# Optimization experiments

Measured on AMD Instinct MI355X. Metric: run time of the kernel, lower is better.

Reference implementation:

```python
import jax, jax.numpy as jnp
import numpy as np

HEADS = 8
DIM_HEAD = 64
WINDOW = 256
CAUSAL = True


def _sliding_window_mask(seq_len: int, window: int, causal: bool) -> jnp.ndarray:
    i = jnp.arange(seq_len)[:, None]
    j = jnp.arange(seq_len)[None, :]
    # attend iff i - window + 1 <= j <= i + window - 1 (end_pos exclusive)
    mask = (j >= i - window + 1) & (j <= i + window - 1)
    if causal:
        mask = mask & (j <= i)
    return mask  # (S, S) bool


def setup_inputs() -> dict:
    key = jax.random.key(0)
    k1, k2, k3 = jax.random.split(key, 3)
    dim = 512
    inner = HEADS * DIM_HEAD
    x = jax.random.normal(k1, (2, 2048, dim), dtype=jnp.float32)
    W_qkv = jax.random.normal(k2, (dim, 3 * inner), dtype=jnp.float32) * 0.02
    W_out = jax.random.normal(k3, (inner, dim), dtype=jnp.float32) * 0.02
    return {"x": x, "W_qkv": W_qkv, "W_out": W_out}


def reference(x, W_qkv, W_out):
    B, S, D = x.shape
    H, Dh = HEADS, DIM_HEAD
    scale = Dh ** (-0.5)
    qkv = x @ W_qkv  # (B, S, 3*H*Dh)
    q, k, v = jnp.split(qkv, 3, axis=-1)
    q = q.reshape(B, S, H, Dh).transpose(0, 2, 1, 3)  # (B, H, S, Dh)
    k = k.reshape(B, S, H, Dh).transpose(0, 2, 1, 3)
    v = v.reshape(B, S, H, Dh).transpose(0, 2, 1, 3)
    scores = jnp.einsum('bhid,bhjd->bhij', q, k) * scale
    mask = _sliding_window_mask(S, WINDOW, CAUSAL)
    mask_value = -jnp.finfo(scores.dtype).max
    scores = jnp.where(mask[None, None, :, :], scores, mask_value)
    attn = jax.nn.softmax(scores, axis=-1)  # (B, H, S, S)
    out = jnp.einsum('bhij,bhjd->bhid', attn, v)
    out = out.transpose(0, 2, 1, 3).reshape(B, S, H * Dh)
    out = out @ W_out  # (B, S, D)
    return (out, attn)
```

## Files before the change

### kernel.cpp

```cpp
#include <hip/hip_runtime.h>
#include <hip/hip_bf16.h>

typedef __bf16 bf16x8 __attribute__((ext_vector_type(8)));
typedef __bf16 bf16x4 __attribute__((ext_vector_type(4)));
typedef float f32x4 __attribute__((ext_vector_type(4)));

#define MFMA16(a,b,c) __builtin_amdgcn_mfma_f32_16x16x32_bf16(a, b, c, 0, 0, 0)

__device__ inline void fill_attn_rows(float* __restrict__ attn, int rowStart, int rowEnd,
                                      int tid) {
  const f32x4 z4 = {0.f, 0.f, 0.f, 0.f};
  for (int g = rowStart; g < rowEnd; g++) {
    const int bh = g >> 11, i = g & 2047;
    const int qt = i >> 6;
    const int lo = qt >= 4 ? (qt - 4) << 6 : 0;
    const int hi = (qt + 1) << 6;
    float* rp = attn + ((size_t)bh << 22) + ((size_t)i << 11);
    for (int j = tid << 2; j < lo; j += 1024)
      __builtin_nontemporal_store(z4, reinterpret_cast<f32x4*>(rp + j));
    for (int j = hi + (tid << 2); j < 2048; j += 1024)
      __builtin_nontemporal_store(z4, reinterpret_cast<f32x4*>(rp + j));
  }
}

__device__ inline void fill_block_chunk(float* __restrict__ attn, int fillStart, int fillEnd,
                                        int fid, int nfill, int tid) {
  const int total = fillEnd - fillStart;
  const int per = (total + nfill - 1) / nfill;
  const int myStart = fillStart + fid * per;
  int myEnd = myStart + per;
  if (myEnd > fillEnd) myEnd = fillEnd;
  if (myStart < myEnd) fill_attn_rows(attn, myStart, myEnd, tid);
}

__device__ inline void transpose_body(const float* __restrict__ in, __bf16* __restrict__ out,
                                      int R, int C, int tile, int tid, float (*t)[65]) {
  const int tilesC = C >> 6;
  const int tc = tile % tilesC, tr = tile / tilesC;
  const int r0 = tr << 6, c0 = tc << 6;
  const int ri = tid >> 2, cq = (tid & 3) << 4;
#pragma unroll
  for (int e = 0; e < 16; e += 4) {
    float4 v = *reinterpret_cast<const float4*>(&in[(size_t)(r0 + ri) * C + c0 + cq + e]);
    t[ri][cq + e]     = v.x;
    t[ri][cq + e + 1] = v.y;
    t[ri][cq + e + 2] = v.z;
    t[ri][cq + e + 3] = v.w;
  }
  __syncthreads();
  const int co = tid >> 2, rq = (tid & 3) << 4;
  __attribute__((aligned(16))) __bf16 buf[16];
#pragma unroll
  for (int e = 0; e < 16; e++) buf[e] = (__bf16)t[rq + e][co];
  *reinterpret_cast<bf16x8*>(&out[(size_t)(c0 + co) * R + r0 + rq])     = *reinterpret_cast<bf16x8*>(&buf[0]);
  *reinterpret_cast<bf16x8*>(&out[(size_t)(c0 + co) * R + r0 + rq + 8]) = *reinterpret_cast<bf16x8*>(&buf[8]);
}

__global__ __launch_bounds__(256) void prep(const float* __restrict__ Wqkv,
                                            const float* __restrict__ Wout,
                                            __bf16* __restrict__ Wqt,
                                            __bf16* __restrict__ Wot) {
  __shared__ float t[64][65];
  const int bid = blockIdx.x, tid = threadIdx.x;
  if (bid < 192) transpose_body(Wqkv, Wqt, 512, 1536, bid, tid, t);
  else           transpose_body(Wout, Wot, 512, 512, bid - 192, tid, t);
}

template <typename AT, typename OT>
__global__ __launch_bounds__(256) void gemm_bt(const AT* __restrict__ A,
                                               const __bf16* __restrict__ Bt,
                                               OT* __restrict__ C, int M, int N, int K,
                                               float* __restrict__ fillAttn,
                                               int fillStart, int fillEnd, int gxCompute) {
  __shared__ __bf16 As[128][72];
  __shared__ __bf16 Bs[128][72];
  const int tid = threadIdx.x;

  if ((int)blockIdx.x >= gxCompute) {
    const int nfx = gridDim.x - gxCompute;
    const int fid = (blockIdx.x - gxCompute) + nfx * blockIdx.y;
    fill_block_chunk(fillAttn, fillStart, fillEnd, fid, nfx * gridDim.y, tid);
    return;
  }

  const int wave = tid >> 6, lane = tid & 63;
  const int c = lane & 15, q4 = lane >> 4;
  const int bm = blockIdx.y << 7, bn = blockIdx.x << 7;
  const int wm = (wave >> 1) << 6, wn = (wave & 1) << 6;
  f32x4 acc[4][4];
#pragma unroll
  for (int m = 0; m < 4; m++)
#pragma unroll
    for (int n = 0; n < 4; n++)
#pragma unroll
      for (int e = 0; e < 4; e++) acc[m][n][e] = 0.f;

  const int srow = tid >> 1, scol = (tid & 1) << 5;
  bf16x8 av[4], bv[4];

  auto loadA = [&](int k0) {
    const AT* ag = A + (size_t)(bm + srow) * K + k0 + scol;
    if constexpr (sizeof(AT) == 4) {
#pragma unroll
      for (int r = 0; r < 4; r++) {
        float4 lo = *reinterpret_cast<const float4*>(ag + r * 8);
        float4 hi = *reinterpret_cast<const float4*>(ag + r * 8 + 4);
        bf16x8 v;
        v[0] = (__bf16)lo.x; v[1] = (__bf16)lo.y; v[2] = (__bf16)lo.z; v[3] = (__bf16)lo.w;
        v[4] = (__bf16)hi.x; v[5] = (__bf16)hi.y; v[6] = (__bf16)hi.z; v[7] = (__bf16)hi.w;
        av[r] = v;
      }
    } else {
#pragma unroll
      for (int r = 0; r < 4; r++) av[r] = *reinterpret_cast<const bf16x8*>(ag + r * 8);
    }
  };
  auto loadB = [&](int k0) {
    const __bf16* bg = Bt + (size_t)(bn + srow) * K + k0 + scol;
#pragma unroll
    for (int r = 0; r < 4; r++) bv[r] = *reinterpret_cast<const bf16x8*>(bg + r * 8);
  };

  loadA(0); loadB(0);
  for (int k0 = 0; k0 < K; k0 += 64) {
    __syncthreads();
#pragma unroll
    for (int r = 0; r < 4; r++) *reinterpret_cast<bf16x8*>(&As[srow][scol + r * 8]) = av[r];
#pragma unroll
    for (int r = 0; r < 4; r++) *reinterpret_cast<bf16x8*>(&Bs[srow][scol + r * 8]) = bv[r];
    __syncthreads();
    if (k0 + 64 < K) { loadA(k0 + 64); loadB(k0 + 64); }
#pragma unroll
    for (int ks = 0; ks < 2; ks++) {
      const int kk = ks * 32 + q4 * 8;
      bf16x8 af[4], bfv[4];
#pragma unroll
      for (int m = 0; m < 4; m++) af[m] = *reinterpret_cast<const bf16x8*>(&As[wm + m * 16 + c][kk]);
#pragma unroll
      for (int n = 0; n < 4; n++) bfv[n] = *reinterpret_cast<const bf16x8*>(&Bs[wn + n * 16 + c][kk]);
#pragma unroll
      for (int m = 0; m < 4; m++)
#pragma unroll
        for (int n = 0; n < 4; n++) acc[m][n] = MFMA16(af[m], bfv[n], acc[m][n]);
    }
  }
#pragma unroll
  for (int m = 0; m < 4; m++)
#pragma unroll
    for (int n = 0; n < 4; n++)
#pragma unroll
      for (int r2 = 0; r2 < 4; r2++) {
        const int row = bm + wm + m * 16 + q4 * 4 + r2;
        const int col = bn + wn + n * 16 + c;
        C[(size_t)row * N + col] = (OT)acc[m][n][r2];
      }
}

__global__ __launch_bounds__(256) void attn_fused(const __bf16* __restrict__ QKV,
                                                  float* __restrict__ attn,
                                                  __bf16* __restrict__ AO) {
  __shared__ __bf16 Qs[64][72];
  __shared__ __bf16 Ks[2][64][72];
  __shared__ __bf16 Ps[2][64][72];
  __shared__ float red[4][64];
  __shared__ float rowstat[64];
  const int tid = threadIdx.x;

  if (blockIdx.x >= 32) {
    const int fid = (blockIdx.x - 32) + (gridDim.x - 32) * blockIdx.y;
    fill_block_chunk(attn, 9000, 25000, fid, (gridDim.x - 32) * gridDim.y, tid);
    return;
  }

  const int qt = blockIdx.x, bh = blockIdx.y;
  const int b = bh >> 3, h = bh & 7;
  const int qi0 = qt << 6;
  const int wave = tid >> 6, lane = tid & 63;
  const int c = lane & 15, q4 = lane >> 4;
  const int base = b * 2048;
  const int r = tid >> 2, qq = (tid & 3) << 4;

  {
    const __bf16* src = QKV + (size_t)(base + qi0 + r) * 1536 + h * 64 + qq;
    *reinterpret_cast<bf16x8*>(&Qs[r][qq]) = *reinterpret_cast<const bf16x8*>(src);
    *reinterpret_cast<bf16x8*>(&Qs[r][qq + 8]) = *reinterpret_cast<const bf16x8*>(src + 8);
  }

  f32x4 acc[5][4];
#pragma unroll
  for (int t = 0; t < 5; t++)
#pragma unroll
    for (int m = 0; m < 4; m++)
#pragma unroll
      for (int e = 0; e < 4; e++) acc[t][m][e] = 0.f;

  const int tfirst = qt >= 4 ? 0 : 4 - qt;
  bf16x8 kv0, kv1;
  {
    const __bf16* s = QKV + (size_t)(base + ((qt - 4 + tfirst) << 6) + r) * 1536 + 512 + h * 64 + qq;
    kv0 = *reinterpret_cast<const bf16x8*>(s);
    kv1 = *reinterpret_cast<const bf16x8*>(s + 8);
  }
  int cur = 0;
#pragma unroll
  for (int t = 0; t < 5; t++) {
    if (qt - 4 + t < 0) continue;
    *reinterpret_cast<bf16x8*>(&Ks[cur][r][qq]) = kv0;
    *reinterpret_cast<bf16x8*>(&Ks[cur][r][qq + 8]) = kv1;
    if (t < 4) {
      const __bf16* s = QKV + (size_t)(base + ((qt - 3 + t) << 6) + r) * 1536 + 512 + h * 64 + qq;
      kv0 = *reinterpret_cast<const bf16x8*>(s);
      kv1 = *reinterpret_cast<const bf16x8*>(s + 8);
    }
    __syncthreads();
#pragma unroll
    for (int ks = 0; ks < 2; ks++) {
      const int kk = ks * 32 + q4 * 8;
      bf16x8 bfr = *reinterpret_cast<const bf16x8*>(&Ks[cur][wave * 16 + c][kk]);
#pragma unroll
      for (int m = 0; m < 4; m++) {
        bf16x8 afr = *reinterpret_cast<const bf16x8*>(&Qs[m * 16 + c][kk]);
        acc[t][m] = MFMA16(afr, bfr, acc[t][m]);
      }
    }
    cur ^= 1;
  }

  const float scale = 0.125f;
#pragma unroll
  for (int t = 0; t < 5; t++) {
    const int jb = ((qt - 4 + t) << 6) + wave * 16 + c;
#pragma unroll
    for (int m = 0; m < 4; m++)
#pragma unroll
      for (int r2 = 0; r2 < 4; r2++) {
        const int ig = qi0 + m * 16 + q4 * 4 + r2;
        const bool valid = (jb >= 0) && (jb <= ig) && (jb >= ig - 255);
        acc[t][m][r2] = valid ? acc[t][m][r2] * scale : -1e30f;
      }
  }

  float pm[16];
#pragma unroll
  for (int m = 0; m < 4; m++)
#pragma unroll
    for (int r2 = 0; r2 < 4; r2++) {
      float v = acc[0][m][r2];
#pragma unroll
      for (int t = 1; t < 5; t++) v = fmaxf(v, acc[t][m][r2]);
      pm[m * 4 + r2] = v;
    }
#pragma unroll
  for (int off = 8; off >= 1; off >>= 1)
#pragma unroll
    for (int i = 0; i < 16; i++) pm[i] = fmaxf(pm[i], __shfl_xor(pm[i], off, 64));
  if (c == 0) {
#pragma unroll
    for (int m = 0; m < 4; m++)
#pragma unroll
      for (int r2 = 0; r2 < 4; r2++) red[wave][m * 16 + q4 * 4 + r2] = pm[m * 4 + r2];
  }
  __syncthreads();
  if (tid < 64)
    rowstat[tid] = fmaxf(fmaxf(red[0][tid], red[1][tid]), fmaxf(red[2][tid], red[3][tid]));
  __syncthreads();

  float rmax[16], ps[16];
#pragma unroll
  for (int m = 0; m < 4; m++)
#pragma unroll
    for (int r2 = 0; r2 < 4; r2++) {
      rmax[m * 4 + r2] = rowstat[m * 16 + q4 * 4 + r2];
      ps[m * 4 + r2] = 0.f;
    }
#pragma unroll
  for (int t = 0; t < 5; t++)
#pragma unroll
    for (int m = 0; m < 4; m++)
#pragma unroll
      for (int r2 = 0; r2 < 4; r2++) {
        float p = __expf(acc[t][m][r2] - rmax[m * 4 + r2]);
        acc[t][m][r2] = p;
        ps[m * 4 + r2] += p;
      }
#pragma unroll
  for (int off = 8; off >= 1; off >>= 1)
#pragma unroll
    for (int i = 0; i < 16; i++) ps[i] += __shfl_xor(ps[i], off, 64);
  if (c == 0) {
#pragma unroll
    for (int m = 0; m < 4; m++)
#pragma unroll
      for (int r2 = 0; r2 < 4; r2++) red[wave][m * 16 + q4 * 4 + r2] = ps[m * 4 + r2];
  }
  __syncthreads();
  if (tid < 64) rowstat[tid] = red[0][tid] + red[1][tid] + red[2][tid] + red[3][tid];
  __syncthreads();

#pragma unroll
  for (int m = 0; m < 4; m++)
#pragma unroll
    for (int r2 = 0; r2 < 4; r2++) {
      const float rinv = 1.0f / rowstat[m * 16 + q4 * 4 + r2];
#pragma unroll
      for (int t = 0; t < 5; t++) acc[t][m][r2] *= rinv;
    }

  f32x4 o[4];
#pragma unroll
  for (int n = 0; n < 4; n++)
#pragma unroll
    for (int e = 0; e < 4; e++) o[n][e] = 0.f;

  const int jv = tid >> 2, dqa = tid & 3;
  bf16x8 vr0, vr1;
  {
    const __bf16* s = QKV + (size_t)(base + ((qt - 4 + tfirst) << 6) + jv) * 1536 + 1024 + h * 64;
    vr0 = *reinterpret_cast<const bf16x8*>(s + dqa * 8);
    vr1 = *reinterpret_cast<const bf16x8*>(s + (dqa + 4) * 8);
  }
  int pcur = 0;
#pragma unroll
  for (int t = 0; t < 5; t++) {
    if (qt - 4 + t < 0) continue;
#pragma unroll
    for (int m = 0; m < 4; m++)
#pragma unroll
      for (int r2 = 0; r2 < 4; r2++)
        Ps[pcur][m * 16 + q4 * 4 + r2][wave * 16 + c] = (__bf16)acc[t][m][r2];
#pragma unroll
    for (int e = 0; e < 8; e++) {
      Ks[pcur][dqa * 8 + e][jv] = vr0[e];
      Ks[pcur][(dqa + 4) * 8 + e][jv] = vr1[e];
    }
    if (t < 4) {
      const __bf16* s = QKV + (size_t)(base + ((qt - 3 + t) << 6) + jv) * 1536 + 1024 + h * 64;
      vr0 = *reinterpret_cast<const bf16x8*>(s + dqa * 8);
      vr1 = *reinterpret_cast<const bf16x8*>(s + (dqa + 4) * 8);
    }
    __syncthreads();
#pragma unroll
    for (int ks = 0; ks < 2; ks++) {
      const int kk = ks * 32 + q4 * 8;
      bf16x8 af = *reinterpret_cast<const bf16x8*>(&Ps[pcur][wave * 16 + c][kk]);
#pragma unroll
      for (int n = 0; n < 4; n++) {
        bf16x8 bfr = *reinterpret_cast<const bf16x8*>(&Ks[pcur][n * 16 + c][kk]);
        o[n] = MFMA16(af, bfr, o[n]);
      }
    }
    pcur ^= 1;
  }

#pragma unroll
  for (int n = 0; n < 4; n++)
#pragma unroll
    for (int r2 = 0; r2 < 4; r2++) {
      const int i = qi0 + wave * 16 + q4 * 4 + r2;
      const int d = n * 16 + c;
      AO[(size_t)(base + i) * 512 + h * 64 + d] = (__bf16)o[n][r2];
    }

  float* arow = attn + ((size_t)bh << 22);
#pragma unroll
  for (int t = 0; t < 5; t++) {
    const int jt0 = (qt - 4 + t) << 6;
    if (jt0 < 0) continue;
    const int jb = jt0 + wave * 16 + c;
#pragma unroll
    for (int m = 0; m < 4; m++)
#pragma unroll
      for (int r2 = 0; r2 < 4; r2++) {
        const int ig = qi0 + m * 16 + q4 * 4 + r2;
        arow[(size_t)ig * 2048 + jb] = acc[t][m][r2];
      }
  }
}

extern "C" void kernel_launch(void* const* d_in, const int* in_sizes, int n_in,
                              void* d_out, int out_size, void* d_ws, size_t ws_size,
                              hipStream_t stream) {
  const float* x = (const float*)d_in[0];
  const float* Wqkv = (const float*)d_in[1];
  const float* Wout = (const float*)d_in[2];
  float* out = (float*)d_out;
  float* attn = out + (size_t)2 * 2048 * 512;

  char* ws = (char*)d_ws;
  __bf16* Wqt  = (__bf16*)(ws);
  __bf16* Wot  = (__bf16*)(ws + 1572864);
  __bf16* QKVb = (__bf16*)(ws + 1572864 + 524288);
  __bf16* AOb  = (__bf16*)(ws + 1572864 + 524288 + 12582912);

  prep<<<256, 256, 0, stream>>>(Wqkv, Wout, Wqt, Wot);

  gemm_bt<float, __bf16><<<dim3(24, 32), 256, 0, stream>>>(x, Wqt, QKVb, 4096, 1536, 512,
                                                           attn, 0, 9000, 12);

  attn_fused<<<dim3(48, 16), 256, 0, stream>>>(QKVb, attn, AOb);

  gemm_bt<__bf16, float><<<dim3(12, 32), 256, 0, stream>>>(AOb, Wot, out, 4096, 512, 512,
                                                           attn, 25000, 32768, 4);
}
```

Before: 87.51 us.

## Fuse all stages into one persistent megakernel with flag-based dependencies

Replaces four separate launches (weight transpose, QKV GEMM, attention, output GEMM) with a single 512-block kernel plus a tiny flag-zeroing kernel. Stages are chained with per-tile atomic counters rather than kernel boundaries. Blocks that are waiting on dependencies pull 16-row chunks of the zero-fill work for the attention matrix from a global work queue. The aim is to remove launch gaps and inter-kernel tail idle time and to overlap the large zero-fill stores with compute, but it depends on all 512 blocks being co-resident (launch bounds of 2 per SM) to avoid deadlock, and spin-waiting adds overhead.

```diff
diff --git a/kernel.cpp b/kernel.cpp
--- a/kernel.cpp
+++ b/kernel.cpp
@@ -2,15 +2,16 @@
 #include <hip/hip_bf16.h>
 
 typedef __bf16 bf16x8 __attribute__((ext_vector_type(8)));
-typedef __bf16 bf16x4 __attribute__((ext_vector_type(4)));
 typedef float f32x4 __attribute__((ext_vector_type(4)));
+typedef __bf16 Row72[72];
 
 #define MFMA16(a,b,c) __builtin_amdgcn_mfma_f32_16x16x32_bf16(a, b, c, 0, 0, 0)
-
-__device__ inline void fill_attn_rows(float* __restrict__ attn, int rowStart, int rowEnd,
-                                      int tid) {
+#define NCH 2048
+
+__device__ inline void fill_chunk(float* __restrict__ attn, int c, int tid) {
   const f32x4 z4 = {0.f, 0.f, 0.f, 0.f};
-  for (int g = rowStart; g < rowEnd; g++) {
+  const int r0 = c << 4;
+  for (int g = r0; g < r0 + 16; g++) {
     const int bh = g >> 11, i = g & 2047;
     const int qt = i >> 6;
     const int lo = qt >= 4 ? (qt - 4) << 6 : 0;
@@ -23,14 +24,52 @@
   }
 }
 
-__device__ inline void fill_block_chunk(float* __restrict__ attn, int fillStart, int fillEnd,
-                                        int fid, int nfill, int tid) {
-  const int total = fillEnd - fillStart;
-  const int per = (total + nfill - 1) / nfill;
-  const int myStart = fillStart + fid * per;
-  int myEnd = myStart + per;
-  if (myEnd > fillEnd) myEnd = fillEnd;
-  if (myStart < myEnd) fill_attn_rows(attn, myStart, myEnd, tid);
+__device__ inline void signal_flag(unsigned* f, int tid) {
+  __syncthreads();
+  if (tid == 0) {
+    __builtin_amdgcn_fence(__ATOMIC_RELEASE, "agent");
+    __hip_atomic_fetch_add(f, 1u, __ATOMIC_RELAXED, __HIP_MEMORY_SCOPE_AGENT);
+  }
+}
+
+__device__ inline void wait_flags_fill(unsigned* flags, int n, unsigned target,
+                                       unsigned* qcnt, float* attn, int* s_state, int tid) {
+  for (;;) {
+    if (tid == 0) {
+      bool ready = true;
+      for (int i = 0; i < n; i++)
+        if (__hip_atomic_load(flags + i, __ATOMIC_RELAXED, __HIP_MEMORY_SCOPE_AGENT) < target) {
+          ready = false; break;
+        }
+      if (ready) *s_state = -1;
+      else {
+        unsigned idx = __hip_atomic_fetch_add(qcnt, 1u, __ATOMIC_RELAXED, __HIP_MEMORY_SCOPE_AGENT);
+        *s_state = idx < NCH ? (int)idx : -2;
+      }
+    }
+    __syncthreads();
+    const int st = *s_state;
+    __syncthreads();
+    if (st == -1) break;
+    if (st >= 0) fill_chunk(attn, st, tid);
+    else __builtin_amdgcn_s_sleep(2);
+  }
+  __builtin_amdgcn_fence(__ATOMIC_ACQUIRE, "agent");
+  __syncthreads();
+}
+
+__device__ inline void drain_fill(unsigned* qcnt, float* attn, int* s_state, int tid) {
+  for (;;) {
+    if (tid == 0) {
+      unsigned idx = __hip_atomic_fetch_add(qcnt, 1u, __ATOMIC_RELAXED, __HIP_MEMORY_SCOPE_AGENT);
+      *s_state = idx < NCH ? (int)idx : -1;
+    }
+    __syncthreads();
+    const int st = *s_state;
+    __syncthreads();
+    if (st < 0) return;
+    fill_chunk(attn, st, tid);
+  }
 }
 
 __device__ inline void transpose_body(const float* __restrict__ in, __bf16* __restrict__ out,
@@ -56,36 +95,14 @@
   *reinterpret_cast<bf16x8*>(&out[(size_t)(c0 + co) * R + r0 + rq + 8]) = *reinterpret_cast<bf16x8*>(&buf[8]);
 }
 
-__global__ __launch_bounds__(256) void prep(const float* __restrict__ Wqkv,
-                                            const float* __restrict__ Wout,
-                                            __bf16* __restrict__ Wqt,
-                                            __bf16* __restrict__ Wot) {
-  __shared__ float t[64][65];
-  const int bid = blockIdx.x, tid = threadIdx.x;
-  if (bid < 192) transpose_body(Wqkv, Wqt, 512, 1536, bid, tid, t);
-  else           transpose_body(Wout, Wot, 512, 512, bid - 192, tid, t);
-}
-
 template <typename AT, typename OT>
-__global__ __launch_bounds__(256) void gemm_bt(const AT* __restrict__ A,
-                                               const __bf16* __restrict__ Bt,
-                                               OT* __restrict__ C, int M, int N, int K,
-                                               float* __restrict__ fillAttn,
-                                               int fillStart, int fillEnd, int gxCompute) {
-  __shared__ __bf16 As[128][72];
-  __shared__ __bf16 Bs[128][72];
-  const int tid = threadIdx.x;
-
-  if ((int)blockIdx.x >= gxCompute) {
-    const int nfx = gridDim.x - gxCompute;
-    const int fid = (blockIdx.x - gxCompute) + nfx * blockIdx.y;
-    fill_block_chunk(fillAttn, fillStart, fillEnd, fid, nfx * gridDim.y, tid);
-    return;
-  }
-
+__device__ inline void gemm_body(const AT* __restrict__ A, const __bf16* __restrict__ Bt,
+                                 OT* __restrict__ C, int M, int N, int K,
+                                 int bm, int bn, char* smem, int tid) {
+  Row72* As = (Row72*)smem;
+  Row72* Bs = (Row72*)(smem + 18432);
   const int wave = tid >> 6, lane = tid & 63;
   const int c = lane & 15, q4 = lane >> 4;
-  const int bm = blockIdx.y << 7, bn = blockIdx.x << 7;
   const int wm = (wave >> 1) << 6, wn = (wave & 1) << 6;
   f32x4 acc[4][4];
 #pragma unroll
@@ -156,23 +173,14 @@
       }
 }
 
-__global__ __launch_bounds__(256) void attn_fused(const __bf16* __restrict__ QKV,
-                                                  float* __restrict__ attn,
-                                                  __bf16* __restrict__ AO) {
-  __shared__ __bf16 Qs[64][72];
-  __shared__ __bf16 Ks[2][64][72];
-  __shared__ __bf16 Ps[2][64][72];
-  __shared__ float red[4][64];
-  __shared__ float rowstat[64];
-  const int tid = threadIdx.x;
-
-  if (blockIdx.x >= 32) {
-    const int fid = (blockIdx.x - 32) + (gridDim.x - 32) * blockIdx.y;
-    fill_block_chunk(attn, 9000, 25000, fid, (gridDim.x - 32) * gridDim.y, tid);
-    return;
-  }
-
-  const int qt = blockIdx.x, bh = blockIdx.y;
+__device__ inline void attn_body(const __bf16* __restrict__ QKV, float* __restrict__ attn,
+                                 __bf16* __restrict__ AO, int qt, int bh, char* smem, int tid) {
+  Row72* Qs = (Row72*)smem;
+  Row72* Ks = (Row72*)(smem + 9216);
+  Row72* Ps = (Row72*)(smem + 27648);
+  float (*red)[64] = (float (*)[64])(smem + 46080);
+  float* rowstat = (float*)(smem + 47104);
+
   const int b = bh >> 3, h = bh & 7;
   const int qi0 = qt << 6;
   const int wave = tid >> 6, lane = tid & 63;
@@ -205,8 +213,8 @@
 #pragma unroll
   for (int t = 0; t < 5; t++) {
     if (qt - 4 + t < 0) continue;
-    *reinterpret_cast<bf16x8*>(&Ks[cur][r][qq]) = kv0;
-    *reinterpret_cast<bf16x8*>(&Ks[cur][r][qq + 8]) = kv1;
+    *reinterpret_cast<bf16x8*>(&Ks[cur * 64 + r][qq]) = kv0;
+    *reinterpret_cast<bf16x8*>(&Ks[cur * 64 + r][qq + 8]) = kv1;
     if (t < 4) {
       const __bf16* s = QKV + (size_t)(base + ((qt - 3 + t) << 6) + r) * 1536 + 512 + h * 64 + qq;
       kv0 = *reinterpret_cast<const bf16x8*>(s);
@@ -216,7 +224,7 @@
 #pragma unroll
     for (int ks = 0; ks < 2; ks++) {
       const int kk = ks * 32 + q4 * 8;
-      bf16x8 bfr = *reinterpret_cast<const bf16x8*>(&Ks[cur][wave * 16 + c][kk]);
+      bf16x8 bfr = *reinterpret_cast<const bf16x8*>(&Ks[cur * 64 + wave * 16 + c][kk]);
 #pragma unroll
       for (int m = 0; m < 4; m++) {
         bf16x8 afr = *reinterpret_cast<const bf16x8*>(&Qs[m * 16 + c][kk]);
@@ -327,11 +335,11 @@
     for (int m = 0; m < 4; m++)
 #pragma unroll
       for (int r2 = 0; r2 < 4; r2++)
-        Ps[pcur][m * 16 + q4 * 4 + r2][wave * 16 + c] = (__bf16)acc[t][m][r2];
+        Ps[pcur * 64 + m * 16 + q4 * 4 + r2][wave * 16 + c] = (__bf16)acc[t][m][r2];
 #pragma unroll
     for (int e = 0; e < 8; e++) {
-      Ks[pcur][dqa * 8 + e][jv] = vr0[e];
-      Ks[pcur][(dqa + 4) * 8 + e][jv] = vr1[e];
+      Ks[pcur * 64 + dqa * 8 + e][jv] = vr0[e];
+      Ks[pcur * 64 + (dqa + 4) * 8 + e][jv] = vr1[e];
     }
     if (t < 4) {
       const __bf16* s = QKV + (size_t)(base + ((qt - 3 + t) << 6) + jv) * 1536 + 1024 + h * 64;
@@ -342,10 +350,10 @@
 #pragma unroll
     for (int ks = 0; ks < 2; ks++) {
       const int kk = ks * 32 + q4 * 8;
-      bf16x8 af = *reinterpret_cast<const bf16x8*>(&Ps[pcur][wave * 16 + c][kk]);
+      bf16x8 af = *reinterpret_cast<const bf16x8*>(&Ps[pcur * 64 + wave * 16 + c][kk]);
 #pragma unroll
       for (int n = 0; n < 4; n++) {
-        bf16x8 bfr = *reinterpret_cast<const bf16x8*>(&Ks[pcur][n * 16 + c][kk]);
+        bf16x8 bfr = *reinterpret_cast<const bf16x8*>(&Ks[pcur * 64 + n * 16 + c][kk]);
         o[n] = MFMA16(af, bfr, o[n]);
       }
     }
@@ -375,6 +383,61 @@
         arow[(size_t)ig * 2048 + jb] = acc[t][m][r2];
       }
   }
+}
+
+__global__ void zero_flags(unsigned* __restrict__ f) {
+  f[threadIdx.x] = 0;
+}
+
+__global__ __launch_bounds__(256, 2) void mega(const float* __restrict__ x,
+                                               const float* __restrict__ Wqkv,
+                                               const float* __restrict__ Wout,
+                                               float* __restrict__ out,
+                                               float* __restrict__ attn,
+                                               __bf16* __restrict__ Wqt,
+                                               __bf16* __restrict__ Wot,
+                                               __bf16* __restrict__ QKVb,
+                                               __bf16* __restrict__ AOb,
+                                               unsigned* __restrict__ flags) {
+  __shared__ __align__(16) char smem[47360];
+  __shared__ int s_state;
+  unsigned* flag0 = flags;
+  unsigned* flag1 = flags + 1;
+  unsigned* flag2 = flags + 33;
+  unsigned* qcnt  = flags + 65;
+  const int id = blockIdx.x, tid = threadIdx.x;
+
+  if (id < 256) {
+    float (*t)[65] = (float (*)[65])smem;
+    if (id < 192) transpose_body(Wqkv, Wqt, 512, 1536, id, tid, t);
+    else          transpose_body(Wout, Wot, 512, 512, id - 192, tid, t);
+    signal_flag(flag0, tid);
+  }
+
+  if (id < 384) {
+    wait_flags_fill(flag0, 1, 256, qcnt, attn, &s_state, tid);
+    gemm_body<float, __bf16>(x, Wqt, QKVb, 4096, 1536, 512,
+                             (id / 12) << 7, (id % 12) << 7, smem, tid);
+    signal_flag(flag1 + id / 12, tid);
+  }
+
+  {
+    const int qt = id >> 4, bh = id & 15;
+    const int b = bh >> 3;
+    const int tlo = (b * 2048 + (qt >= 4 ? qt - 4 : 0) * 64) >> 7;
+    const int thi = (b * 2048 + qt * 64 + 63) >> 7;
+    wait_flags_fill(flag1 + tlo, thi - tlo + 1, 12, qcnt, attn, &s_state, tid);
+    attn_body(QKVb, attn, AOb, qt, bh, smem, tid);
+    signal_flag(flag2 + b * 16 + (qt >> 1), tid);
+  }
+
+  if (id < 128) {
+    wait_flags_fill(flag2 + (id >> 2), 1, 16, qcnt, attn, &s_state, tid);
+    gemm_body<__bf16, float>(AOb, Wot, out, 4096, 512, 512,
+                             (id >> 2) << 7, (id & 3) << 7, smem, tid);
+  }
+
+  drain_fill(qcnt, attn, &s_state, tid);
 }
 
 extern "C" void kernel_launch(void* const* d_in, const int* in_sizes, int n_in,
@@ -389,16 +452,10 @@
   char* ws = (char*)d_ws;
   __bf16* Wqt  = (__bf16*)(ws);
   __bf16* Wot  = (__bf16*)(ws + 1572864);
-  __bf16* QKVb = (__bf16*)(ws + 1572864 + 524288);
-  __bf16* AOb  = (__bf16*)(ws + 1572864 + 524288 + 12582912);
-
-  prep<<<256, 256, 0, stream>>>(Wqkv, Wout, Wqt, Wot);
-
-  gemm_bt<float, __bf16><<<dim3(24, 32), 256, 0, stream>>>(x, Wqt, QKVb, 4096, 1536, 512,
-                                                           attn, 0, 9000, 12);
-
-  attn_fused<<<dim3(48, 16), 256, 0, stream>>>(QKVb, attn, AOb);
-
-  gemm_bt<__bf16, float><<<dim3(12, 32), 256, 0, stream>>>(AOb, Wot, out, 4096, 512, 512,
-                                                           attn, 25000, 32768, 4);
-}
+  __bf16* QKVb = (__bf16*)(ws + 2097152);
+  __bf16* AOb  = (__bf16*)(ws + 14680064);
+  unsigned* flags = (unsigned*)(ws + 18874368);
+
+  zero_flags<<<1, 128, 0, stream>>>(flags);
+  mega<<<512, 256, 0, stream>>>(x, Wqkv, Wout, out, attn, Wqt, Wot, QKVb, AOb, flags);
+}
```

New measurement: 173.5 us. 1.98x slower.

## Assign query rows per wave so softmax reduces within wave

Applied to the files above, without the earlier changes.

Each wave now owns 16 query rows across all 64 key columns, not 16 key columns across all query rows. Row max and row sum therefore need only intra-wave shuffles, which removes the shared-memory reduction arrays and four block barriers. Q fragments are held in registers instead of LDS, and P is staged in a per-wave buffer rather than a shared double buffer. The attention-write store pattern changes too: each wave now writes 16 rows across 64 columns instead of 64 rows across 16 columns.

```diff
diff --git a/kernel.cpp b/kernel.cpp
--- a/kernel.cpp
+++ b/kernel.cpp
@@ -2,7 +2,6 @@
 #include <hip/hip_bf16.h>
 
 typedef __bf16 bf16x8 __attribute__((ext_vector_type(8)));
-typedef __bf16 bf16x4 __attribute__((ext_vector_type(4)));
 typedef float f32x4 __attribute__((ext_vector_type(4)));
 
 #define MFMA16(a,b,c) __builtin_amdgcn_mfma_f32_16x16x32_bf16(a, b, c, 0, 0, 0)
@@ -159,11 +158,8 @@
 __global__ __launch_bounds__(256) void attn_fused(const __bf16* __restrict__ QKV,
                                                   float* __restrict__ attn,
                                                   __bf16* __restrict__ AO) {
-  __shared__ __bf16 Qs[64][72];
-  __shared__ __bf16 Ks[2][64][72];
-  __shared__ __bf16 Ps[2][64][72];
-  __shared__ float red[4][64];
-  __shared__ float rowstat[64];
+  __shared__ __bf16 KV[2][64][72];
+  __shared__ __bf16 Pw[4][16][72];
   const int tid = threadIdx.x;
 
   if (blockIdx.x >= 32) {
@@ -180,19 +176,20 @@
   const int base = b * 2048;
   const int r = tid >> 2, qq = (tid & 3) << 4;
 
+  bf16x8 qf0, qf1;
   {
-    const __bf16* src = QKV + (size_t)(base + qi0 + r) * 1536 + h * 64 + qq;
-    *reinterpret_cast<bf16x8*>(&Qs[r][qq]) = *reinterpret_cast<const bf16x8*>(src);
-    *reinterpret_cast<bf16x8*>(&Qs[r][qq + 8]) = *reinterpret_cast<const bf16x8*>(src + 8);
+    const __bf16* s = QKV + (size_t)(base + qi0 + wave * 16 + c) * 1536 + h * 64 + q4 * 8;
+    qf0 = *reinterpret_cast<const bf16x8*>(s);
+    qf1 = *reinterpret_cast<const bf16x8*>(s + 32);
   }
 
   f32x4 acc[5][4];
 #pragma unroll
   for (int t = 0; t < 5; t++)
 #pragma unroll
-    for (int m = 0; m < 4; m++)
-#pragma unroll
-      for (int e = 0; e < 4; e++) acc[t][m][e] = 0.f;
+    for (int ct = 0; ct < 4; ct++)
+#pragma unroll
+      for (int e = 0; e < 4; e++) acc[t][ct][e] = 0.f;
 
   const int tfirst = qt >= 4 ? 0 : 4 - qt;
   bf16x8 kv0, kv1;
@@ -205,8 +202,8 @@
 #pragma unroll
   for (int t = 0; t < 5; t++) {
     if (qt - 4 + t < 0) continue;
-    *reinterpret_cast<bf16x8*>(&Ks[cur][r][qq]) = kv0;
-    *reinterpret_cast<bf16x8*>(&Ks[cur][r][qq + 8]) = kv1;
+    *reinterpret_cast<bf16x8*>(&KV[cur][r][qq]) = kv0;
+    *reinterpret_cast<bf16x8*>(&KV[cur][r][qq + 8]) = kv1;
     if (t < 4) {
       const __bf16* s = QKV + (size_t)(base + ((qt - 3 + t) << 6) + r) * 1536 + 512 + h * 64 + qq;
       kv0 = *reinterpret_cast<const bf16x8*>(s);
@@ -216,95 +213,73 @@
 #pragma unroll
     for (int ks = 0; ks < 2; ks++) {
       const int kk = ks * 32 + q4 * 8;
-      bf16x8 bfr = *reinterpret_cast<const bf16x8*>(&Ks[cur][wave * 16 + c][kk]);
-#pragma unroll
-      for (int m = 0; m < 4; m++) {
-        bf16x8 afr = *reinterpret_cast<const bf16x8*>(&Qs[m * 16 + c][kk]);
-        acc[t][m] = MFMA16(afr, bfr, acc[t][m]);
+      const bf16x8 af = ks ? qf1 : qf0;
+#pragma unroll
+      for (int ct = 0; ct < 4; ct++) {
+        bf16x8 bfr = *reinterpret_cast<const bf16x8*>(&KV[cur][ct * 16 + c][kk]);
+        acc[t][ct] = MFMA16(af, bfr, acc[t][ct]);
       }
     }
     cur ^= 1;
   }
 
   const float scale = 0.125f;
+  const int igBase = qi0 + wave * 16 + q4 * 4;
 #pragma unroll
   for (int t = 0; t < 5; t++) {
-    const int jb = ((qt - 4 + t) << 6) + wave * 16 + c;
-#pragma unroll
-    for (int m = 0; m < 4; m++)
+#pragma unroll
+    for (int ct = 0; ct < 4; ct++) {
+      const int jb = ((qt - 4 + t) << 6) + ct * 16 + c;
 #pragma unroll
       for (int r2 = 0; r2 < 4; r2++) {
-        const int ig = qi0 + m * 16 + q4 * 4 + r2;
+        const int ig = igBase + r2;
         const bool valid = (jb >= 0) && (jb <= ig) && (jb >= ig - 255);
-        acc[t][m][r2] = valid ? acc[t][m][r2] * scale : -1e30f;
-      }
-  }
-
-  float pm[16];
-#pragma unroll
-  for (int m = 0; m < 4; m++)
-#pragma unroll
-    for (int r2 = 0; r2 < 4; r2++) {
-      float v = acc[0][m][r2];
-#pragma unroll
-      for (int t = 1; t < 5; t++) v = fmaxf(v, acc[t][m][r2]);
-      pm[m * 4 + r2] = v;
-    }
+        acc[t][ct][r2] = valid ? acc[t][ct][r2] * scale : -1e30f;
+      }
+    }
+  }
+
+  float pm[4];
+#pragma unroll
+  for (int r2 = 0; r2 < 4; r2++) {
+    float v = acc[0][0][r2];
+#pragma unroll
+    for (int t = 0; t < 5; t++)
+#pragma unroll
+      for (int ct = 0; ct < 4; ct++) v = fmaxf(v, acc[t][ct][r2]);
+    pm[r2] = v;
+  }
 #pragma unroll
   for (int off = 8; off >= 1; off >>= 1)
 #pragma unroll
-    for (int i = 0; i < 16; i++) pm[i] = fmaxf(pm[i], __shfl_xor(pm[i], off, 64));
-  if (c == 0) {
-#pragma unroll
-    for (int m = 0; m < 4; m++)
-#pragma unroll
-      for (int r2 = 0; r2 < 4; r2++) red[wave][m * 16 + q4 * 4 + r2] = pm[m * 4 + r2];
-  }
+    for (int r2 = 0; r2 < 4; r2++) pm[r2] = fmaxf(pm[r2], __shfl_xor(pm[r2], off, 64));
+
+  float ps[4] = {0.f, 0.f, 0.f, 0.f};
+#pragma unroll
+  for (int t = 0; t < 5; t++)
+#pragma unroll
+    for (int ct = 0; ct < 4; ct++)
+#pragma unroll
+      for (int r2 = 0; r2 < 4; r2++) {
+        float p = __expf(acc[t][ct][r2] - pm[r2]);
+        acc[t][ct][r2] = p;
+        ps[r2] += p;
+      }
+#pragma unroll
+  for (int off = 8; off >= 1; off >>= 1)
+#pragma unroll
+    for (int r2 = 0; r2 < 4; r2++) ps[r2] += __shfl_xor(ps[r2], off, 64);
+
+#pragma unroll
+  for (int r2 = 0; r2 < 4; r2++) ps[r2] = 1.0f / ps[r2];
+#pragma unroll
+  for (int t = 0; t < 5; t++)
+#pragma unroll
+    for (int ct = 0; ct < 4; ct++)
+#pragma unroll
+      for (int r2 = 0; r2 < 4; r2++) acc[t][ct][r2] *= ps[r2];
+
   __syncthreads();
-  if (tid < 64)
-    rowstat[tid] = fmaxf(fmaxf(red[0][tid], red[1][tid]), fmaxf(red[2][tid], red[3][tid]));
-  __syncthreads();
-
-  float rmax[16], ps[16];
-#pragma unroll
-  for (int m = 0; m < 4; m++)
-#pragma unroll
-    for (int r2 = 0; r2 < 4; r2++) {
-      rmax[m * 4 + r2] = rowstat[m * 16 + q4 * 4 + r2];
-      ps[m * 4 + r2] = 0.f;
-    }
-#pragma unroll
-  for (int t = 0; t < 5; t++)
-#pragma unroll
-    for (int m = 0; m < 4; m++)
-#pragma unroll
-      for (int r2 = 0; r2 < 4; r2++) {
-        float p = __expf(acc[t][m][r2] - rmax[m * 4 + r2]);
-        acc[t][m][r2] = p;
-        ps[m * 4 + r2] += p;
-      }
-#pragma unroll
-  for (int off = 8; off >= 1; off >>= 1)
-#pragma unroll
-    for (int i = 0; i < 16; i++) ps[i] += __shfl_xor(ps[i], off, 64);
-  if (c == 0) {
-#pragma unroll
-    for (int m = 0; m < 4; m++)
-#pragma unroll
-      for (int r2 = 0; r2 < 4; r2++) red[wave][m * 16 + q4 * 4 + r2] = ps[m * 4 + r2];
-  }
-  __syncthreads();
-  if (tid < 64) rowstat[tid] = red[0][tid] + red[1][tid] + red[2][tid] + red[3][tid];
-  __syncthreads();
-
-#pragma unroll
-  for (int m = 0; m < 4; m++)
-#pragma unroll
-    for (int r2 = 0; r2 < 4; r2++) {
-      const float rinv = 1.0f / rowstat[m * 16 + q4 * 4 + r2];
-#pragma unroll
-      for (int t = 0; t < 5; t++) acc[t][m][r2] *= rinv;
-    }
 
   f32x4 o[4];
 #pragma unroll
@@ -324,14 +299,14 @@
   for (int t = 0; t < 5; t++) {
     if (qt - 4 + t < 0) continue;
 #pragma unroll
-    for (int m = 0; m < 4; m++)
+    for (int ct = 0; ct < 4; ct++)
 #pragma unroll
       for (int r2 = 0; r2 < 4; r2++)
-        Ps[pcur][m * 16 + q4 * 4 + r2][wave * 16 + c] = (__bf16)acc[t][m][r2];
+        Pw[wave][q4 * 4 + r2][ct * 16 + c] = (__bf16)acc[t][ct][r2];
 #pragma unroll
     for (int e = 0; e < 8; e++) {
-      Ks[pcur][dqa * 8 + e][jv] = vr0[e];
-      Ks[pcur][(dqa + 4) * 8 + e][jv] = vr1[e];
+      KV[pcur][dqa * 8 + e][jv] = vr0[e];
+      KV[pcur][(dqa + 4) * 8 + e][jv] = vr1[e];
     }
     if (t < 4) {
       const __bf16* s = QKV + (size_t)(base + ((qt - 3 + t) << 6) + jv) * 1536 + 1024 + h * 64;
@@ -342,10 +317,10 @@
 #pragma unroll
     for (int ks = 0; ks < 2; ks++) {
       const int kk = ks * 32 + q4 * 8;
-      bf16x8 af = *reinterpret_cast<const bf16x8*>(&Ps[pcur][wave * 16 + c][kk]);
+      bf16x8 af = *reinterpret_cast<const bf16x8*>(&Pw[wave][c][kk]);
 #pragma unroll
       for (int n = 0; n < 4; n++) {
-        bf16x8 bfr = *reinterpret_cast<const bf16x8*>(&Ks[pcur][n * 16 + c][kk]);
+        bf16x8 bfr = *reinterpret_cast<const bf16x8*>(&KV[pcur][n * 16 + c][kk]);
         o[n] = MFMA16(af, bfr, o[n]);
       }
     }
@@ -356,7 +331,7 @@
   for (int n = 0; n < 4; n++)
 #pragma unroll
     for (int r2 = 0; r2 < 4; r2++) {
-      const int i = qi0 + wave * 16 + q4 * 4 + r2;
+      const int i = igBase + r2;
       const int d = n * 16 + c;
       AO[(size_t)(base + i) * 512 + h * 64 + d] = (__bf16)o[n][r2];
     }
@@ -366,14 +341,15 @@
   for (int t = 0; t < 5; t++) {
     const int jt0 = (qt - 4 + t) << 6;
     if (jt0 < 0) continue;
-    const int jb = jt0 + wave * 16 + c;
-#pragma unroll
-    for (int m = 0; m < 4; m++)
+#pragma unroll
+    for (int ct = 0; ct < 4; ct++) {
+      const int jb = jt0 + ct * 16 + c;
 #pragma unroll
       for (int r2 = 0; r2 < 4; r2++) {
-        const int ig = qi0 + m * 16 + q4 * 4 + r2;
-        arow[(size_t)ig * 2048 + jb] = acc[t][m][r2];
-      }
+        const int ig = igBase + r2;
+        arow[(size_t)ig * 2048 + jb] = acc[t][ct][r2];
+      }
+    }
   }
 }
 
```

Measured after the change: 84.70 us. -3.2%, faster.
